# Optimization experiments

Hardware: AMD Instinct MI355X
Metric: run time of the kernel (lower is better)

The kernel has to match this reference:

```python
import jax, jax.numpy as jnp
import numpy as np

H = 8  # num_heads


def _ln(x, g, b):
    mu = x.mean(-1, keepdims=True)
    var = ((x - mu) ** 2).mean(-1, keepdims=True)
    return (x - mu) * jax.lax.rsqrt(var + 1e-5) * g + b


def setup_inputs() -> dict:
    key = jax.random.key(0)
    ks = jax.random.split(key, 24)
    B, N, V, E, D, R, L = 8, 512, 50000, 300, 256, 100, 4
    dh = D // H
    s = 0.02
    inp = {}
    inp['token_ids'] = jax.random.randint(ks[0], (B, N), 0, V, dtype=jnp.int32)
    inp['relations'] = jax.random.randint(ks[1], (B, N, N), 0, R, dtype=jnp.int32)
    m = jax.random.bernoulli(ks[2], 0.9, (B, N, N))
    eye = jnp.eye(N, dtype=bool)[None]
    inp['relations_mask'] = jnp.logical_or(m, eye)  # keep diagonal valid so every row attends somewhere
    inp['embed'] = jax.random.normal(ks[3], (V, E), jnp.float32) * s
    inp['W_in'] = jax.random.normal(ks[4], (E, D), jnp.float32) * s
    inp['b_in'] = jnp.zeros((D,), jnp.float32)
    inp['Wq'] = jax.random.normal(ks[5], (L, D, D), jnp.float32) * s
    inp['Wk'] = jax.random.normal(ks[6], (L, D, D), jnp.float32) * s
    inp['Wv'] = jax.random.normal(ks[7], (L, D, D), jnp.float32) * s
    inp['Wo'] = jax.random.normal(ks[8], (L, D, D), jnp.float32) * s
    inp['ln1_g'] = jnp.ones((L, D), jnp.float32)
    inp['ln1_b'] = jnp.zeros((L, D), jnp.float32)
    inp['ln2_g'] = jnp.ones((L, D), jnp.float32)
    inp['ln2_b'] = jnp.zeros((L, D), jnp.float32)
    inp['W1'] = jax.random.normal(ks[9], (L, D, 4 * D), jnp.float32) * s
    inp['b1'] = jnp.zeros((L, 4 * D), jnp.float32)
    inp['W2'] = jax.random.normal(ks[10], (L, 4 * D, D), jnp.float32) * s
    inp['b2'] = jnp.zeros((L, D), jnp.float32)
    inp['rel_k_emb'] = jax.random.normal(ks[11], (R, dh), jnp.float32) * s
    inp['rel_v_emb'] = jax.random.normal(ks[12], (R, dh), jnp.float32) * s
    inp['W_out'] = jax.random.normal(ks[13], (D, D), jnp.float32) * s
    inp['b_out'] = jnp.zeros((D,), jnp.float32)
    return inp


def reference(token_ids, relations, relations_mask, embed, W_in, b_in, Wq, Wk, Wv, Wo,
              ln1_g, ln1_b, ln2_g, ln2_b, W1, b1, W2, b2, rel_k_emb, rel_v_emb, W_out, b_out):
    # Input layer: embedding lookup + projection to gnn hidden size.
    x = embed[token_ids]                          # [B,N,E]
    x = jax.nn.relu(x @ W_in + b_in)              # [B,N,D]
    B, N, D = x.shape
    dh = D // H
    # Shared relation embeddings (share_layers=True, share_heads=True): gathered once.
    rk = rel_k_emb[relations]                     # [B,N,N,dh]
    rv = rel_v_emb[relations]                     # [B,N,N,dh]
    neg = jnp.asarray(-1e9, x.dtype)
    scale = jnp.asarray(1.0 / np.sqrt(dh), x.dtype)
    L = Wq.shape[0]
    for l in range(L):  # fixed small layer count
        q = (x @ Wq[l]).reshape(B, N, H, dh).transpose(0, 2, 1, 3)
        k = (x @ Wk[l]).reshape(B, N, H, dh).transpose(0, 2, 1, 3)
        v = (x @ Wv[l]).reshape(B, N, H, dh).transpose(0, 2, 1, 3)
        # Relation-aware scores: q.k + q.r_k (RAT-SQL)
        scores = (jnp.einsum('bhnd,bhmd->bhnm', q, k)
                  + jnp.einsum('bhnd,bnmd->bhnm', q, rk)) * scale
        scores = jnp.where(relations_mask[:, None], scores, neg)
        a = jax.nn.softmax(scores, axis=-1)       # [B,H,N,N]
        z = (jnp.einsum('bhnm,bhmd->bhnd', a, v)
             + jnp.einsum('bhnm,bnmd->bhnd', a, rv))
        z = z.transpose(0, 2, 1, 3).reshape(B, N, D) @ Wo[l]
        x = _ln(x + z, ln1_g[l], ln1_b[l])
        f = jax.nn.relu(x @ W1[l] + b1[l]) @ W2[l] + b2[l]
        x = _ln(x + f, ln2_g[l], ln2_b[l])
    # Output layer projection
    return x @ W_out + b_out
```

## Files before the change

kernel.cpp:

```cpp
#include <hip/hip_runtime.h>
#include <hip/hip_bf16.h>

#define NTOK 4096
#define NN   512

typedef __attribute__((ext_vector_type(8))) short bf16x8;
typedef __attribute__((ext_vector_type(4))) float f32x4;
typedef __attribute__((ext_vector_type(4))) unsigned short u16x4;

__device__ __forceinline__ float bf16_to_f(unsigned short u) {
    unsigned int x = ((unsigned int)u) << 16;
    return __builtin_bit_cast(float, x);
}
__device__ __forceinline__ unsigned short f_to_bf16(float f) {
    unsigned int b = __builtin_bit_cast(unsigned int, f);
    return (unsigned short)((b + 0x7fff + ((b >> 16) & 1)) >> 16);
}
__device__ __forceinline__ bf16x8 pack8(float4 a, float4 b) {
    bf16x8 v;
    v[0]=(short)f_to_bf16(a.x); v[1]=(short)f_to_bf16(a.y);
    v[2]=(short)f_to_bf16(a.z); v[3]=(short)f_to_bf16(a.w);
    v[4]=(short)f_to_bf16(b.x); v[5]=(short)f_to_bf16(b.y);
    v[6]=(short)f_to_bf16(b.z); v[7]=(short)f_to_bf16(b.w);
    return v;
}

__global__ void detect_mask_kernel(const unsigned char* __restrict__ m, int* __restrict__ flag) {
    __shared__ int f;
    if (threadIdx.x == 0) f = 0;
    __syncthreads();
    int any = 0;
    for (int i = threadIdx.x; i < 4096; i += 256) {
        if ((i & 3) != 0 && m[i] != 0) any = 1;
    }
    if (any) atomicOr(&f, 1);
    __syncthreads();
    if (threadIdx.x == 0) *flag = f;
}

__global__ __launch_bounds__(256) void prep_rel16(
    const int* __restrict__ rel, const void* __restrict__ mask,
    const int* __restrict__ flag, short* __restrict__ rel16)
{
    const bool mbyte = (*flag != 0);
    const unsigned char* m8 = (const unsigned char*)mask;
    const int* m32 = (const int*)mask;
    const int i = (blockIdx.x * 256 + threadIdx.x) * 2;
    int2 rv = *(const int2*)(rel + i);
    int ok0, ok1;
    if (mbyte) { ok0 = m8[i]; ok1 = m8[i + 1]; }
    else       { ok0 = (m32[i] != 0); ok1 = (m32[i + 1] != 0); }
    short2 o;
    o.x = ok0 ? (short)rv.x : (short)-1;
    o.y = ok1 ? (short)rv.y : (short)-1;
    *(short2*)(rel16 + i) = o;
}

__global__ __launch_bounds__(256) void tcast256(
    const float* __restrict__ Wq, const float* __restrict__ Wk,
    const float* __restrict__ Wv, const float* __restrict__ Wo,
    const float* __restrict__ Wout, unsigned short* __restrict__ wt,
    int nL, float scale)
{
    const int z = blockIdx.z;
    const float* src; unsigned short* dst; float sc = 1.f;
    if (z >= nL * 4) {
        src = Wout; dst = wt + (size_t)nL * 786432;
    } else {
        const int l = z >> 2, which = z & 3;
        if      (which == 0) { src = Wq + (size_t)l * 65536; sc = scale; }
        else if (which == 1) { src = Wk + (size_t)l * 65536; }
        else if (which == 2) { src = Wv + (size_t)l * 65536; }
        else                 { src = Wo + (size_t)l * 65536; }
        dst = wt + (size_t)l * 786432 + which * 65536;
    }
    __shared__ float tile[32][33];
    const int t = threadIdx.x, tx = t & 31, ty = t >> 5;
    const int n0 = blockIdx.x * 32, k0 = blockIdx.y * 32;
#pragma unroll
    for (int p = 0; p < 4; ++p)
        tile[ty + p * 8][tx] = src[(size_t)(k0 + ty + p * 8) * 256 + n0 + tx];
    __syncthreads();
#pragma unroll
    for (int p = 0; p < 4; ++p)
        dst[(size_t)(n0 + ty + p * 8) * 256 + k0 + tx] = f_to_bf16(tile[tx][ty + p * 8] * sc);
}

__global__ __launch_bounds__(256) void tcastKN(
    const float* __restrict__ in, unsigned short* __restrict__ out,
    int K, int N, long inStride, long outStride)
{
    in  += (size_t)blockIdx.z * inStride;
    out += (size_t)blockIdx.z * outStride;
    __shared__ float tile[32][33];
    const int t = threadIdx.x, tx = t & 31, ty = t >> 5;
    const int n0 = blockIdx.x * 32, k0 = blockIdx.y * 32;
#pragma unroll
    for (int p = 0; p < 4; ++p)
        tile[ty + p * 8][tx] = in[(size_t)(k0 + ty + p * 8) * N + n0 + tx];
    __syncthreads();
#pragma unroll
    for (int p = 0; p < 4; ++p)
        out[(size_t)(n0 + ty + p * 8) * K + k0 + tx] = f_to_bf16(tile[tx][ty + p * 8]);
}

__global__ __launch_bounds__(256) void embed_proj_kernel(
    const int* __restrict__ tok, const float* __restrict__ embed,
    const float* __restrict__ W_in, const float* __restrict__ b_in,
    float* __restrict__ x, unsigned short* __restrict__ xh)
{
    __shared__ float emb[8][304];
    __shared__ int tloc[8];
    const int t = threadIdx.x;
    const int r0 = blockIdx.x * 8;
    if (t < 8) tloc[t] = tok[r0 + t];
    __syncthreads();
    for (int i = t; i < 8 * 300; i += 256) {
        int r = i / 300, e = i - r * 300;
        emb[r][e] = embed[(size_t)tloc[r] * 300 + e];
    }
    __syncthreads();
    float acc[8] = {0.f,0.f,0.f,0.f,0.f,0.f,0.f,0.f};
    const int d = t;
    for (int e = 0; e < 300; ++e) {
        float w = W_in[e * 256 + d];
#pragma unroll
        for (int r = 0; r < 8; ++r) acc[r] += emb[r][e] * w;
    }
    const float bb = b_in[d];
#pragma unroll
    for (int r = 0; r < 8; ++r) {
        float o = acc[r] + bb;
        o = o > 0.f ? o : 0.f;
        x[(size_t)(r0 + r) * 256 + d] = o;
        xh[(size_t)(r0 + r) * 256 + d] = f_to_bf16(o);
    }
}

__global__ __launch_bounds__(256) void gemm_bigk64(
    const unsigned short* __restrict__ A, const unsigned short* __restrict__ WT,
    const float* __restrict__ bias, float* __restrict__ Cf, unsigned short* __restrict__ Ch,
    int M, int K, int Nc, int relu)
{
    __shared__ unsigned short As[64][256];
    __shared__ unsigned short Bs[64][256];
    char* Ab = (char*)As; char* Bb = (char*)Bs;
    const int t = threadIdx.x;
    const int lane = t & 63, w = t >> 6;
    const int g = lane >> 4, li = lane & 15;
    const int r0 = blockIdx.y * 64, c0 = blockIdx.x * 64;

    f32x4 acc[4];
#pragma unroll
    for (int i = 0; i < 4; ++i) acc[i] = (f32x4){0.f,0.f,0.f,0.f};

    for (int k0 = 0; k0 < K; k0 += 256) {
        if (k0) __syncthreads();
#pragma unroll
        for (int j = 0; j < 8; ++j) {
            int idx = j * 256 + t;
            int row = idx >> 5;
            int colb = (idx & 31) * 16;
            int sw = row * 512 + (colb ^ ((row & 7) << 4));
            *(bf16x8*)(Ab + sw) = *(const bf16x8*)(A  + (size_t)(r0 + row) * K + k0 + (idx & 31) * 8);
            *(bf16x8*)(Bb + sw) = *(const bf16x8*)(WT + (size_t)(c0 + row) * K + k0 + (idx & 31) * 8);
        }
        __syncthreads();
        const int arow = 16 * w + li;
        const int xr = (li & 7) << 4;
#pragma unroll
        for (int ks = 0; ks < 8; ++ks) {
            const int kb = (g * 8 + ks * 32) * 2;
            bf16x8 af = *(const bf16x8*)(Ab + arow * 512 + (kb ^ xr));
#pragma unroll
            for (int sub = 0; sub < 4; ++sub) {
                const int brow = sub * 16 + li;
                bf16x8 bfr = *(const bf16x8*)(Bb + brow * 512 + (kb ^ xr));
                acc[sub] = __builtin_amdgcn_mfma_f32_16x16x32_bf16(af, bfr, acc[sub], 0, 0, 0);
            }
        }
    }
#pragma unroll
    for (int sub = 0; sub < 4; ++sub) {
        int col = c0 + sub * 16 + li;
        float bv = bias ? bias[col] : 0.f;
#pragma unroll
        for (int r = 0; r < 4; ++r) {
            int row = r0 + 16 * w + g * 4 + r;
            float o = acc[sub][r] + bv;
            if (relu) o = fmaxf(o, 0.f);
            if (Ch) Ch[(size_t)row * Nc + col] = f_to_bf16(o);
            else    Cf[(size_t)row * Nc + col] = o;
        }
    }
}

__global__ __launch_bounds__(256) void gemm_bigk32(
    const unsigned short* __restrict__ A, const unsigned short* __restrict__ WT,
    const float* __restrict__ bias, float* __restrict__ Cf, unsigned short* __restrict__ Ch,
    int M, int K, int Nc, int relu)
{
    __shared__ unsigned short As[32][256];
    __shared__ unsigned short Bs[64][256];
    char* Ab = (char*)As; char* Bb = (char*)Bs;
    const int t = threadIdx.x;
    const int lane = t & 63, w = t >> 6;
    const int g = lane >> 4, li = lane & 15;
    const int r0 = blockIdx.y * 32, c0 = blockIdx.x * 64;

    f32x4 acc[2];
    acc[0] = (f32x4){0.f,0.f,0.f,0.f};
    acc[1] = (f32x4){0.f,0.f,0.f,0.f};

    for (int k0 = 0; k0 < K; k0 += 256) {
        if (k0) __syncthreads();
#pragma unroll
        for (int j = 0; j < 4; ++j) {
            int idx = j * 256 + t;
            int row = idx >> 5;
            int colb = (idx & 31) * 16;
            int sw = row * 512 + (colb ^ ((row & 7) << 4));
            *(bf16x8*)(Ab + sw) = *(const bf16x8*)(A + (size_t)(r0 + row) * K + k0 + (idx & 31) * 8);
        }
#pragma unroll
        for (int j = 0; j < 8; ++j) {
            int idx = j * 256 + t;
            int row = idx >> 5;
            int colb = (idx & 31) * 16;
            int sw = row * 512 + (colb ^ ((row & 7) << 4));
            *(bf16x8*)(Bb + sw) = *(const bf16x8*)(WT + (size_t)(c0 + row) * K + k0 + (idx & 31) * 8);
        }
        __syncthreads();
        const int arow = 16 * (w & 1) + li;
        const int xr = (li & 7) << 4;
#pragma unroll
        for (int ks = 0; ks < 8; ++ks) {
            const int kb = (g * 8 + ks * 32) * 2;
            bf16x8 af = *(const bf16x8*)(Ab + arow * 512 + (kb ^ xr));
#pragma unroll
            for (int sub = 0; sub < 2; ++sub) {
                const int brow = (w >> 1) * 32 + sub * 16 + li;
                bf16x8 bfr = *(const bf16x8*)(Bb + brow * 512 + (kb ^ xr));
                acc[sub] = __builtin_amdgcn_mfma_f32_16x16x32_bf16(af, bfr, acc[sub], 0, 0, 0);
            }
        }
    }
#pragma unroll
    for (int sub = 0; sub < 2; ++sub) {
        int col = c0 + (w >> 1) * 32 + sub * 16 + li;
        float bv = bias ? bias[col] : 0.f;
#pragma unroll
        for (int r = 0; r < 4; ++r) {
            int row = r0 + 16 * (w & 1) + g * 4 + r;
            float o = acc[sub][r] + bv;
            if (relu) o = fmaxf(o, 0.f);
            if (Ch) Ch[(size_t)row * Nc + col] = f_to_bf16(o);
            else    Cf[(size_t)row * Nc + col] = o;
        }
    }
}

__global__ __launch_bounds__(256) void qrk_kernel(
    const unsigned short* __restrict__ qkvh, const float* __restrict__ relk_g,
    unsigned short* __restrict__ qrkg)
{
    const int n0 = blockIdx.x * 64, h = blockIdx.y, b = blockIdx.z;
    const int t = threadIdx.x, lane = t & 63, w = t >> 6;
    const int g = lane >> 4, li = lane & 15;
    const int qrow = 16 * w + g * 4;

    __shared__ unsigned short relk_s[100][40];
    for (int i = t; i < 400; i += 256) {
        int rr = i >> 2, d8 = (i & 3) * 8;
        const float* sp = relk_g + rr * 32 + d8;
        *(bf16x8*)&relk_s[rr][d8] = pack8(*(const float4*)sp, *(const float4*)(sp + 4));
    }
    bf16x8 qf = *(const bf16x8*)(qkvh + (size_t)(b * NN + n0 + 16 * w + li) * 768 + h * 32 + g * 8);
    __syncthreads();
#pragma unroll
    for (int rc = 0; rc < 7; ++rc) {
        bf16x8 bb = *(const bf16x8*)&relk_s[rc * 16 + li][g * 8];
        f32x4 s = __builtin_amdgcn_mfma_f32_16x16x32_bf16(qf, bb, (f32x4){0.f,0.f,0.f,0.f}, 0, 0, 0);
        int col = rc * 16 + li;
        if (col < 100) {
#pragma unroll
            for (int r = 0; r < 4; ++r)
                qrkg[((size_t)(b * 8 + h) * NN + n0 + qrow + r) * 100 + col] = f_to_bf16(s[r]);
        }
    }
}

__global__ __launch_bounds__(256, 4) void attn_mfma(
    const unsigned short* __restrict__ qkvh,
    const short* __restrict__ rel16,
    const unsigned short* __restrict__ qrkg,
    const float* __restrict__ relv_g,
    float* __restrict__ zpart, float* __restrict__ smpart)
{
    const int p = blockIdx.x;
    const int cx = p & 7, k = p >> 3;
    const int sg = cx * 16 + (k >> 3);
    const int h  = k & 7;
    const int b = sg >> 4, chunk = sg & 15;
    const int n0 = chunk * 32;

    const int t = threadIdx.x;
    const int lane = t & 63, w = t >> 6;
    const int qw = w & 1, mhalf = w >> 1;
    const int g = lane >> 4, li = lane & 15;
    const int qrow = 16 * qw + g * 4;
    const int mbase = mhalf * 256;

    __shared__ float wrel[32][100];
    __shared__ unsigned short qrk_lds[32][100];
    __shared__ union {
        unsigned short relvT[32][136];
        struct {
            unsigned short v_t[2][2][32][40];
            unsigned short p_s[4][16][40];
        } mn;
    } u;

    for (int i = t; i < 3200; i += 256) ((float*)wrel)[i] = 0.f;
    {
        const unsigned short* qsrc = qrkg + ((size_t)(b * 8 + h) * NN + n0) * 100;
        for (int i = t; i < 1600; i += 256) {
            int row = i / 50, off = (i - row * 50) * 2;
            *(unsigned int*)&qrk_lds[row][off] =
                *(const unsigned int*)(qsrc + (size_t)row * 100 + off);
        }
    }
    bf16x8 qf = *(const bf16x8*)(qkvh + (size_t)(b * NN + n0 + 16 * qw + li) * 768 + h * 32 + g * 8);

    const short* relrow[4];
#pragma unroll
    for (int r = 0; r < 4; ++r)
        relrow[r] = rel16 + ((size_t)b * NN + n0 + qrow + r) * NN;
    const int th = t & 127;
    const int vm = th & 31, vdg = th >> 5;
    const size_t kRB = (size_t)(b * NN) * 768 + 256 + h * 32 + g * 8;
    const size_t vRB = (size_t)(b * NN) * 768 + 512 + h * 32 + vdg * 8;

    bf16x8 kbuf[2][2]; bf16x8 vbuf[2]; short rbuf[2][8];
#pragma unroll
    for (int i = 0; i < 8; ++i)
        rbuf[0][i] = relrow[i & 3][mbase + (i >> 2) * 16 + li];
    kbuf[0][0] = *(const bf16x8*)(qkvh + kRB + (size_t)(mbase + li) * 768);
    kbuf[0][1] = *(const bf16x8*)(qkvh + kRB + (size_t)(mbase + 16 + li) * 768);
    vbuf[0]    = *(const bf16x8*)(qkvh + vRB + (size_t)(mbase + vm) * 768);

    float smacc[4] = {0.f, 0.f, 0.f, 0.f};
    f32x4 zf[2];
    zf[0] = (f32x4){0.f,0.f,0.f,0.f};
    zf[1] = (f32x4){0.f,0.f,0.f,0.f};

#pragma unroll
    for (int tt = 0; tt < 8; ++tt) {
        const int cur = tt & 1, nxt = cur ^ 1;
        {
            bf16x8 vv = vbuf[cur];
#pragma unroll
            for (int j = 0; j < 8; ++j)
                u.mn.v_t[mhalf][cur][vdg * 8 + j][vm] = (unsigned short)vv[j];
        }
        if (tt + 1 < 8) {
            const int m0n = mbase + (tt + 1) * 32;
#pragma unroll
            for (int i = 0; i < 8; ++i)
                rbuf[nxt][i] = relrow[i & 3][m0n + (i >> 2) * 16 + li];
        }
        __syncthreads();
        bf16x8 kf0 = kbuf[cur][0], kf1 = kbuf[cur][1];
        if (tt + 1 < 8) {
            const int m0n = mbase + (tt + 1) * 32;
            kbuf[nxt][0] = *(const bf16x8*)(qkvh + kRB + (size_t)(m0n + li) * 768);
            kbuf[nxt][1] = *(const bf16x8*)(qkvh + kRB + (size_t)(m0n + 16 + li) * 768);
            vbuf[nxt]    = *(const bf16x8*)(qkvh + vRB + (size_t)(m0n + vm) * 768);
        }
        f32x4 s0 = __builtin_amdgcn_mfma_f32_16x16x32_bf16(qf, kf0, (f32x4){0.f,0.f,0.f,0.f}, 0, 0, 0);
        f32x4 s1 = __builtin_amdgcn_mfma_f32_16x16x32_bf16(qf, kf1, (f32x4){0.f,0.f,0.f,0.f}, 0, 0, 0);
        float pr[8];
#pragma unroll
        for (int i = 0; i < 8; ++i) {
            const int r = i & 3;
            const int rl = rbuf[cur][i];
            const float qadd = bf16_to_f(qrk_lds[qrow + r][rl < 0 ? 0 : rl]);
            const float sv = ((i >> 2) ? s1[r] : s0[r]) + qadd;
            float pv = 0.f;
            if (rl >= 0) {
                pv = __expf(fminf(sv, 50.f));
                atomicAdd(&wrel[qrow + r][rl], pv);
            }
            smacc[r] += pv;
            pr[i] = pv;
        }
#pragma unroll
        for (int i = 0; i < 8; ++i)
            u.mn.p_s[w][g * 4 + (i & 3)][(i >> 2) * 16 + li] = f_to_bf16(pr[i]);
        asm volatile("s_waitcnt lgkmcnt(0)" ::: "memory");
        __builtin_amdgcn_sched_barrier(0);
        bf16x8 pa = *(const bf16x8*)&u.mn.p_s[w][li][g * 8];
#pragma unroll
        for (int dc = 0; dc < 2; ++dc) {
            bf16x8 vb = *(const bf16x8*)&u.mn.v_t[mhalf][cur][dc * 16 + li][g * 8];
            zf[dc] = __builtin_amdgcn_mfma_f32_16x16x32_bf16(pa, vb, zf[dc], 0, 0, 0);
        }
    }
    __syncthreads();

    for (int i = t; i < 32 * 36; i += 256) {
        int d = i / 36, c = 100 + (i - (i / 36) * 36);
        u.relvT[d][c] = 0;
    }
    for (int i = t; i < 400; i += 256) {
        int rr2 = i >> 2, d8 = (i & 3) * 8;
        const float* sp = relv_g + rr2 * 32 + d8;
        float4 s0 = *(const float4*)sp, s1 = *(const float4*)(sp + 4);
        u.relvT[d8 + 0][rr2] = f_to_bf16(s0.x);
        u.relvT[d8 + 1][rr2] = f_to_bf16(s0.y);
        u.relvT[d8 + 2][rr2] = f_to_bf16(s0.z);
        u.relvT[d8 + 3][rr2] = f_to_bf16(s0.w);
        u.relvT[d8 + 4][rr2] = f_to_bf16(s1.x);
        u.relvT[d8 + 5][rr2] = f_to_bf16(s1.y);
        u.relvT[d8 + 6][rr2] = f_to_bf16(s1.z);
        u.relvT[d8 + 7][rr2] = f_to_bf16(s1.w);
    }
    __syncthreads();
    if (mhalf == 0) {
#pragma unroll
        for (int kc = 0; kc < 4; ++kc) {
            const int kbase = kc * 32 + g * 8;
            const float* wp = &wrel[16 * qw + li][0];
            bf16x8 af;
#pragma unroll
            for (int j = 0; j < 8; ++j) {
                int id = kbase + j;
                float val = (id < 100) ? wp[id] : 0.f;
                af[j] = (short)f_to_bf16(val);
            }
#pragma unroll
            for (int dc = 0; dc < 2; ++dc) {
                bf16x8 vbr = *(const bf16x8*)&u.relvT[dc * 16 + li][kbase];
                zf[dc] = __builtin_amdgcn_mfma_f32_16x16x32_bf16(af, vbr, zf[dc], 0, 0, 0);
            }
        }
    }
#pragma unroll
    for (int r = 0; r < 4; ++r) {
        smacc[r] += __shfl_xor(smacc[r], 1, 64);
        smacc[r] += __shfl_xor(smacc[r], 2, 64);
        smacc[r] += __shfl_xor(smacc[r], 4, 64);
        smacc[r] += __shfl_xor(smacc[r], 8, 64);
    }
#pragma unroll
    for (int r = 0; r < 4; ++r) {
        const int row = b * NN + n0 + qrow + r;
        size_t ob = (size_t)mhalf * 1048576 + (size_t)row * 256 + h * 32;
#pragma unroll
        for (int dc = 0; dc < 2; ++dc)
            zpart[ob + dc * 16 + li] = zf[dc][r];
        if (li == 0)
            smpart[(size_t)mhalf * 32768 + (size_t)row * 8 + h] = smacc[r];
    }
}

__global__ __launch_bounds__(256) void combine_kernel(
    const float* __restrict__ zpart, const float* __restrict__ smpart,
    unsigned short* __restrict__ zbf)
{
    const int t = threadIdx.x;
    const int wi = t >> 6, lane = t & 63;
    const int row = blockIdx.x * 4 + wi;
    const int h = lane >> 3;
    float den = 0.f;
    float4 acc = make_float4(0.f, 0.f, 0.f, 0.f);
#pragma unroll
    for (int s = 0; s < 2; ++s) {
        den += smpart[(size_t)s * 32768 + (size_t)row * 8 + h];
        float4 v = *(const float4*)(zpart + (size_t)s * 1048576 + (size_t)row * 256 + lane * 4);
        acc.x += v.x; acc.y += v.y; acc.z += v.z; acc.w += v.w;
    }
    const float inv = 1.f / den;
    u16x4 oh;
    oh[0] = f_to_bf16(acc.x * inv);
    oh[1] = f_to_bf16(acc.y * inv);
    oh[2] = f_to_bf16(acc.z * inv);
    oh[3] = f_to_bf16(acc.w * inv);
    *(u16x4*)(zbf + (size_t)row * 256 + lane * 4) = oh;
}

__global__ __launch_bounds__(256) void ln_kernel(
    const float* __restrict__ xin, const float* __restrict__ y,
    const float* __restrict__ g, const float* __restrict__ bsh,
    float* __restrict__ xout, unsigned short* __restrict__ xh)
{
    const int t = threadIdx.x;
    const int w = t >> 6, lane = t & 63;
    const size_t row = (size_t)blockIdx.x * 4 + w;
    const float4 xv = *(const float4*)(xin + row * 256 + lane * 4);
    const float4 yv = *(const float4*)(y + row * 256 + lane * 4);
    float4 sv;
    sv.x = xv.x + yv.x; sv.y = xv.y + yv.y; sv.z = xv.z + yv.z; sv.w = xv.w + yv.w;
    float sum = sv.x + sv.y + sv.z + sv.w;
    float sq  = sv.x * sv.x + sv.y * sv.y + sv.z * sv.z + sv.w * sv.w;
#pragma unroll
    for (int off = 1; off < 64; off <<= 1) {
        sum += __shfl_xor(sum, off, 64);
        sq  += __shfl_xor(sq, off, 64);
    }
    const float mu = sum * (1.f / 256.f);
    const float var = sq * (1.f / 256.f) - mu * mu;
    const float rs = rsqrtf(var + 1e-5f);
    const float4 gv = *(const float4*)(g + lane * 4);
    const float4 bv = *(const float4*)(bsh + lane * 4);
    float4 o;
    o.x = (sv.x - mu) * rs * gv.x + bv.x;
    o.y = (sv.y - mu) * rs * gv.y + bv.y;
    o.z = (sv.z - mu) * rs * gv.z + bv.z;
    o.w = (sv.w - mu) * rs * gv.w + bv.w;
    *(float4*)(xout + row * 256 + lane * 4) = o;
    u16x4 oh;
    oh[0] = f_to_bf16(o.x); oh[1] = f_to_bf16(o.y);
    oh[2] = f_to_bf16(o.z); oh[3] = f_to_bf16(o.w);
    *(u16x4*)(xh + row * 256 + lane * 4) = oh;
}

extern "C" void kernel_launch(void* const* d_in, const int* in_sizes, int n_in,
                              void* d_out, int out_size, void* d_ws, size_t ws_size,
                              hipStream_t stream)
{
    (void)in_sizes; (void)n_in; (void)out_size;
    const int*   tok   = (const int*)d_in[0];
    const int*   rel   = (const int*)d_in[1];
    const void*  mask  = d_in[2];
    const float* embed = (const float*)d_in[3];
    const float* W_in  = (const float*)d_in[4];
    const float* b_in  = (const float*)d_in[5];
    const float* Wq    = (const float*)d_in[6];
    const float* Wk    = (const float*)d_in[7];
    const float* Wv    = (const float*)d_in[8];
    const float* Wo    = (const float*)d_in[9];
    const float* ln1g  = (const float*)d_in[10];
    const float* ln1b  = (const float*)d_in[11];
    const float* ln2g  = (const float*)d_in[12];
    const float* ln2b  = (const float*)d_in[13];
    const float* W1    = (const float*)d_in[14];
    const float* b1    = (const float*)d_in[15];
    const float* W2    = (const float*)d_in[16];
    const float* b2    = (const float*)d_in[17];
    const float* relk  = (const float*)d_in[18];
    const float* relv  = (const float*)d_in[19];
    const float* Wout  = (const float*)d_in[20];
    const float* bout  = (const float*)d_in[21];
    float* out = (float*)d_out;
    const float scale = 0.17677669529663687f;

    float* ws = (float*)d_ws;
    float*          x     = ws;
    unsigned short* xh    = (unsigned short*)(ws + 1048576);
    unsigned short* zbf   = (unsigned short*)(ws + 1572864);
    float*          zo    = ws + 2097152;
    unsigned short* qkvh  = (unsigned short*)(ws + 3145728);
    unsigned short* hbh   = (unsigned short*)(ws + 4718592);
    float*          zpart = ws + 6815744;
    float*          smpart= ws + 8912896;
    unsigned short* qrkg  = (unsigned short*)(ws + 8978432);
    int*            flag  = (int*)(ws + 10616832);
    unsigned short* wt    = (unsigned short*)(ws + 10616848);

    const size_t wsf = ws_size >> 2;
    const bool tierA = wsf >= 13271100;
    short* rel16 = tierA ? (short*)(ws + 12222480) : (short*)hbh;

    detect_mask_kernel<<<1, 256, 0, stream>>>((const unsigned char*)mask, flag);
    embed_proj_kernel<<<512, 256, 0, stream>>>(tok, embed, W_in, b_in, x, xh);
    if (tierA) {
        prep_rel16<<<4096, 256, 0, stream>>>(rel, mask, flag, rel16);
        tcast256<<<dim3(8, 8, 17), 256, 0, stream>>>(Wq, Wk, Wv, Wo, Wout, wt, 4, scale);
        tcastKN<<<dim3(32, 8, 4), 256, 0, stream>>>(W1, wt + 262144, 256, 1024, 262144, 786432);
        tcastKN<<<dim3(8, 32, 4), 256, 0, stream>>>(W2, wt + 524288, 1024, 256, 262144, 786432);
    }

    for (int l = 0; l < 4; ++l) {
        unsigned short* wl = tierA ? wt + (size_t)l * 786432 : wt;
        if (!tierA) {
            prep_rel16<<<4096, 256, 0, stream>>>(rel, mask, flag, rel16);
            tcast256<<<dim3(8, 8, 4), 256, 0, stream>>>(
                Wq + (size_t)l * 65536, Wk + (size_t)l * 65536,
                Wv + (size_t)l * 65536, Wo + (size_t)l * 65536, Wout, wt, 1, scale);
            tcastKN<<<dim3(32, 8, 1), 256, 0, stream>>>(W1 + (size_t)l * 262144, wt + 262144, 256, 1024, 0, 0);
            tcastKN<<<dim3(8, 32, 1), 256, 0, stream>>>(W2 + (size_t)l * 262144, wt + 524288, 1024, 256, 0, 0);
        }
        gemm_bigk64<<<dim3(12, 64), 256, 0, stream>>>(xh, wl, nullptr, nullptr, qkvh,
                                                      NTOK, 256, 768, 0);
        qrk_kernel<<<dim3(8, 8, 8), 256, 0, stream>>>(qkvh, relk, qrkg);
        attn_mfma<<<1024, 256, 0, stream>>>(qkvh, rel16, qrkg, relv, zpart, smpart);
        combine_kernel<<<1024, 256, 0, stream>>>(zpart, smpart, zbf);
        gemm_bigk32<<<dim3(4, 128), 256, 0, stream>>>(zbf, wl + 196608, nullptr, zo, nullptr,
                                                      NTOK, 256, 256, 0);
        ln_kernel<<<1024, 256, 0, stream>>>(x, zo, ln1g + l * 256, ln1b + l * 256, x, xh);
        gemm_bigk64<<<dim3(16, 64), 256, 0, stream>>>(xh, wl + 262144, b1 + l * 1024, nullptr, hbh,
                                                      NTOK, 256, 1024, 1);
        gemm_bigk32<<<dim3(4, 128), 256, 0, stream>>>(hbh, wl + 524288, b2 + l * 256, zo, nullptr,
                                                      NTOK, 1024, 256, 0);
        ln_kernel<<<1024, 256, 0, stream>>>(x, zo, ln2g + l * 256, ln2b + l * 256, x, xh);
    }
    unsigned short* woutT = wt;
    if (tierA) {
        woutT = wt + (size_t)4 * 786432;
    } else {
        tcast256<<<dim3(8, 8, 1), 256, 0, stream>>>(Wq, Wk, Wv, Wo, Wout, wt, 0, scale);
    }
    gemm_bigk32<<<dim3(4, 128), 256, 0, stream>>>(xh, woutT, bout, out, nullptr,
                                                  NTOK, 256, 256, 0);
}
```

Measured before the change: 623.5 us.

## Fold q·relk into QKV GEMM via precomputed Wq·relkᵀ and fuse combine into Wo GEMM

Precomputes per-layer weight columns Wq_h·rel_kᵀ so the QKV projection GEMM directly emits the q·r_k scores (widened output to 1600 columns), removing the separate qrk kernel. The partial-softmax combine step is fused into a new Wo GEMM that reads zpart/smpart, normalizes, and packs to bf16 in LDS, removing the combine kernel and its zbf round trip. This trades two launches and intermediate buffers for a wider GEMM (more FLOPs and a larger strided qkv buffer) and extra bf16 rounding of the folded weights.

```diff
diff --git a/kernel.cpp b/kernel.cpp
--- a/kernel.cpp
+++ b/kernel.cpp
@@ -3,6 +3,8 @@
 
 #define NTOK 4096
 #define NN   512
+#define QST  1600
+#define LSTR 999424
 
 typedef __attribute__((ext_vector_type(8))) short bf16x8;
 typedef __attribute__((ext_vector_type(4))) float f32x4;
@@ -65,14 +67,15 @@
     const int z = blockIdx.z;
     const float* src; unsigned short* dst; float sc = 1.f;
     if (z >= nL * 4) {
-        src = Wout; dst = wt + (size_t)nL * 786432;
+        src = Wout; dst = wt + (size_t)nL * LSTR;
     } else {
         const int l = z >> 2, which = z & 3;
-        if      (which == 0) { src = Wq + (size_t)l * 65536; sc = scale; }
-        else if (which == 1) { src = Wk + (size_t)l * 65536; }
-        else if (which == 2) { src = Wv + (size_t)l * 65536; }
-        else                 { src = Wo + (size_t)l * 65536; }
-        dst = wt + (size_t)l * 786432 + which * 65536;
+        size_t off;
+        if      (which == 0) { src = Wq + (size_t)l * 65536; sc = scale; off = 0; }
+        else if (which == 1) { src = Wk + (size_t)l * 65536; off = 65536; }
+        else if (which == 2) { src = Wv + (size_t)l * 65536; off = 131072; }
+        else                 { src = Wo + (size_t)l * 65536; off = 409600; }
+        dst = wt + (size_t)l * LSTR + off;
     }
     __shared__ float tile[32][33];
     const int t = threadIdx.x, tx = t & 31, ty = t >> 5;
@@ -102,6 +105,32 @@
 #pragma unroll
     for (int p = 0; p < 4; ++p)
         out[(size_t)(n0 + ty + p * 8) * K + k0 + tx] = f_to_bf16(tile[tx][ty + p * 8]);
+}
+
+__global__ __launch_bounds__(256) void wqr_kernel(
+    unsigned short* __restrict__ wt, const float* __restrict__ relk_g, long lstride)
+{
+    const int h = blockIdx.x, t = threadIdx.x;
+    unsigned short* wl = wt + (size_t)blockIdx.y * lstride;
+    unsigned short* out = wl + 196608;
+    if (h == 8) {
+#pragma unroll
+        for (int i = 0; i < 32; ++i) out[(size_t)(800 + i) * 256 + t] = 0;
+        return;
+    }
+    __shared__ float rk[100][32];
+    for (int i = t; i < 3200; i += 256) rk[i >> 5][i & 31] = relk_g[i];
+    float wq_e[32];
+#pragma unroll
+    for (int d = 0; d < 32; ++d)
+        wq_e[d] = bf16_to_f(wl[(size_t)(h * 32 + d) * 256 + t]);
+    __syncthreads();
+    for (int r = 0; r < 100; ++r) {
+        float acc = 0.f;
+#pragma unroll
+        for (int d = 0; d < 32; ++d) acc += wq_e[d] * rk[r][d];
+        out[(size_t)(h * 100 + r) * 256 + t] = f_to_bf16(acc);
+    }
 }
 
 __global__ __launch_bounds__(256) void embed_proj_kernel(
@@ -260,40 +289,83 @@
     }
 }
 
-__global__ __launch_bounds__(256) void qrk_kernel(
-    const unsigned short* __restrict__ qkvh, const float* __restrict__ relk_g,
-    unsigned short* __restrict__ qrkg)
-{
-    const int n0 = blockIdx.x * 64, h = blockIdx.y, b = blockIdx.z;
-    const int t = threadIdx.x, lane = t & 63, w = t >> 6;
+__global__ __launch_bounds__(256) void gemm_wo(
+    const float* __restrict__ zpart, const float* __restrict__ smpart,
+    const unsigned short* __restrict__ WT, float* __restrict__ Cf, int Nc)
+{
+    __shared__ unsigned short As[32][256];
+    __shared__ unsigned short Bs[64][256];
+    __shared__ float den[32][8];
+    char* Ab = (char*)As; char* Bb = (char*)Bs;
+    const int t = threadIdx.x;
+    const int lane = t & 63, w = t >> 6;
     const int g = lane >> 4, li = lane & 15;
-    const int qrow = 16 * w + g * 4;
-
-    __shared__ unsigned short relk_s[100][40];
-    for (int i = t; i < 400; i += 256) {
-        int rr = i >> 2, d8 = (i & 3) * 8;
-        const float* sp = relk_g + rr * 32 + d8;
-        *(bf16x8*)&relk_s[rr][d8] = pack8(*(const float4*)sp, *(const float4*)(sp + 4));
-    }
-    bf16x8 qf = *(const bf16x8*)(qkvh + (size_t)(b * NN + n0 + 16 * w + li) * 768 + h * 32 + g * 8);
-    __syncthreads();
-#pragma unroll
-    for (int rc = 0; rc < 7; ++rc) {
-        bf16x8 bb = *(const bf16x8*)&relk_s[rc * 16 + li][g * 8];
-        f32x4 s = __builtin_amdgcn_mfma_f32_16x16x32_bf16(qf, bb, (f32x4){0.f,0.f,0.f,0.f}, 0, 0, 0);
-        int col = rc * 16 + li;
-        if (col < 100) {
-#pragma unroll
-            for (int r = 0; r < 4; ++r)
-                qrkg[((size_t)(b * 8 + h) * NN + n0 + qrow + r) * 100 + col] = f_to_bf16(s[r]);
+    const int r0 = blockIdx.y * 32, c0 = blockIdx.x * 64;
+
+    {
+        int row = t >> 3, h2 = t & 7;
+        float s = smpart[(size_t)(r0 + row) * 8 + h2] +
+                  smpart[32768 + (size_t)(r0 + row) * 8 + h2];
+        den[row][h2] = 1.f / s;
+    }
+    __syncthreads();
+#pragma unroll
+    for (int j = 0; j < 4; ++j) {
+        int idx = j * 256 + t;
+        int row = idx >> 5;
+        int k8 = (idx & 31) * 8;
+        const float* z0 = zpart + (size_t)(r0 + row) * 256 + k8;
+        const float* z1 = z0 + 1048576;
+        float4 a0 = *(const float4*)z0, a1 = *(const float4*)(z0 + 4);
+        float4 b0 = *(const float4*)z1, b1 = *(const float4*)(z1 + 4);
+        float dv = den[row][k8 >> 5];
+        a0.x = (a0.x + b0.x) * dv; a0.y = (a0.y + b0.y) * dv;
+        a0.z = (a0.z + b0.z) * dv; a0.w = (a0.w + b0.w) * dv;
+        a1.x = (a1.x + b1.x) * dv; a1.y = (a1.y + b1.y) * dv;
+        a1.z = (a1.z + b1.z) * dv; a1.w = (a1.w + b1.w) * dv;
+        int colb = (idx & 31) * 16;
+        int sw = row * 512 + (colb ^ ((row & 7) << 4));
+        *(bf16x8*)(Ab + sw) = pack8(a0, a1);
+    }
+#pragma unroll
+    for (int j = 0; j < 8; ++j) {
+        int idx = j * 256 + t;
+        int row = idx >> 5;
+        int colb = (idx & 31) * 16;
+        int sw = row * 512 + (colb ^ ((row & 7) << 4));
+        *(bf16x8*)(Bb + sw) = *(const bf16x8*)(WT + (size_t)(c0 + row) * 256 + (idx & 31) * 8);
+    }
+    __syncthreads();
+    f32x4 acc[2];
+    acc[0] = (f32x4){0.f,0.f,0.f,0.f};
+    acc[1] = (f32x4){0.f,0.f,0.f,0.f};
+    const int arow = 16 * (w & 1) + li;
+    const int xr = (li & 7) << 4;
+#pragma unroll
+    for (int ks = 0; ks < 8; ++ks) {
+        const int kb = (g * 8 + ks * 32) * 2;
+        bf16x8 af = *(const bf16x8*)(Ab + arow * 512 + (kb ^ xr));
+#pragma unroll
+        for (int sub = 0; sub < 2; ++sub) {
+            const int brow = (w >> 1) * 32 + sub * 16 + li;
+            bf16x8 bfr = *(const bf16x8*)(Bb + brow * 512 + (kb ^ xr));
+            acc[sub] = __builtin_amdgcn_mfma_f32_16x16x32_bf16(af, bfr, acc[sub], 0, 0, 0);
+        }
+    }
+#pragma unroll
+    for (int sub = 0; sub < 2; ++sub) {
+        int col = c0 + (w >> 1) * 32 + sub * 16 + li;
+#pragma unroll
+        for (int r = 0; r < 4; ++r) {
+            int row = r0 + 16 * (w & 1) + g * 4 + r;
+            Cf[(size_t)row * Nc + col] = acc[sub][r];
         }
     }
 }
 
 __global__ __launch_bounds__(256, 4) void attn_mfma(
-    const unsigned short* __restrict__ qkvh,
+    const unsigned short* __restrict__ qkvg,
     const short* __restrict__ rel16,
-    const unsigned short* __restrict__ qrkg,
     const float* __restrict__ relv_g,
     float* __restrict__ zpart, float* __restrict__ smpart)
 {
@@ -323,14 +395,14 @@
 
     for (int i = t; i < 3200; i += 256) ((float*)wrel)[i] = 0.f;
     {
-        const unsigned short* qsrc = qrkg + ((size_t)(b * 8 + h) * NN + n0) * 100;
+        const unsigned short* qsrc = qkvg + (size_t)(b * NN + n0) * QST + 768 + h * 100;
         for (int i = t; i < 1600; i += 256) {
             int row = i / 50, off = (i - row * 50) * 2;
             *(unsigned int*)&qrk_lds[row][off] =
-                *(const unsigned int*)(qsrc + (size_t)row * 100 + off);
-        }
-    }
-    bf16x8 qf = *(const bf16x8*)(qkvh + (size_t)(b * NN + n0 + 16 * qw + li) * 768 + h * 32 + g * 8);
+                *(const unsigned int*)(qsrc + (size_t)row * QST + off);
+        }
+    }
+    bf16x8 qf = *(const bf16x8*)(qkvg + (size_t)(b * NN + n0 + 16 * qw + li) * QST + h * 32 + g * 8);
 
     const short* relrow[4];
 #pragma unroll
@@ -338,16 +410,16 @@
         relrow[r] = rel16 + ((size_t)b * NN + n0 + qrow + r) * NN;
     const int th = t & 127;
     const int vm = th & 31, vdg = th >> 5;
-    const size_t kRB = (size_t)(b * NN) * 768 + 256 + h * 32 + g * 8;
-    const size_t vRB = (size_t)(b * NN) * 768 + 512 + h * 32 + vdg * 8;
+    const size_t kRB = (size_t)(b * NN) * QST + 256 + h * 32 + g * 8;
+    const size_t vRB = (size_t)(b * NN) * QST + 512 + h * 32 + vdg * 8;
 
     bf16x8 kbuf[2][2]; bf16x8 vbuf[2]; short rbuf[2][8];
 #pragma unroll
     for (int i = 0; i < 8; ++i)
         rbuf[0][i] = relrow[i & 3][mbase + (i >> 2) * 16 + li];
-    kbuf[0][0] = *(const bf16x8*)(qkvh + kRB + (size_t)(mbase + li) * 768);
-    kbuf[0][1] = *(const bf16x8*)(qkvh + kRB + (size_t)(mbase + 16 + li) * 768);
-    vbuf[0]    = *(const bf16x8*)(qkvh + vRB + (size_t)(mbase + vm) * 768);
+    kbuf[0][0] = *(const bf16x8*)(qkvg + kRB + (size_t)(mbase + li) * QST);
+    kbuf[0][1] = *(const bf16x8*)(qkvg + kRB + (size_t)(mbase + 16 + li) * QST);
+    vbuf[0]    = *(const bf16x8*)(qkvg + vRB + (size_t)(mbase + vm) * QST);
 
     float smacc[4] = {0.f, 0.f, 0.f, 0.f};
     f32x4 zf[2];
@@ -373,9 +445,9 @@
         bf16x8 kf0 = kbuf[cur][0], kf1 = kbuf[cur][1];
         if (tt + 1 < 8) {
             const int m0n = mbase + (tt + 1) * 32;
-            kbuf[nxt][0] = *(const bf16x8*)(qkvh + kRB + (size_t)(m0n + li) * 768);
-            kbuf[nxt][1] = *(const bf16x8*)(qkvh + kRB + (size_t)(m0n + 16 + li) * 768);
-            vbuf[nxt]    = *(const bf16x8*)(qkvh + vRB + (size_t)(m0n + vm) * 768);
+            kbuf[nxt][0] = *(const bf16x8*)(qkvg + kRB + (size_t)(m0n + li) * QST);
+            kbuf[nxt][1] = *(const bf16x8*)(qkvg + kRB + (size_t)(m0n + 16 + li) * QST);
+            vbuf[nxt]    = *(const bf16x8*)(qkvg + vRB + (size_t)(m0n + vm) * QST);
         }
         f32x4 s0 = __builtin_amdgcn_mfma_f32_16x16x32_bf16(qf, kf0, (f32x4){0.f,0.f,0.f,0.f}, 0, 0, 0);
         f32x4 s1 = __builtin_amdgcn_mfma_f32_16x16x32_bf16(qf, kf1, (f32x4){0.f,0.f,0.f,0.f}, 0, 0, 0);
@@ -462,31 +534,6 @@
         if (li == 0)
             smpart[(size_t)mhalf * 32768 + (size_t)row * 8 + h] = smacc[r];
     }
-}
-
-__global__ __launch_bounds__(256) void combine_kernel(
-    const float* __restrict__ zpart, const float* __restrict__ smpart,
-    unsigned short* __restrict__ zbf)
-{
-    const int t = threadIdx.x;
-    const int wi = t >> 6, lane = t & 63;
-    const int row = blockIdx.x * 4 + wi;
-    const int h = lane >> 3;
-    float den = 0.f;
-    float4 acc = make_float4(0.f, 0.f, 0.f, 0.f);
-#pragma unroll
-    for (int s = 0; s < 2; ++s) {
-        den += smpart[(size_t)s * 32768 + (size_t)row * 8 + h];
-        float4 v = *(const float4*)(zpart + (size_t)s * 1048576 + (size_t)row * 256 + lane * 4);
-        acc.x += v.x; acc.y += v.y; acc.z += v.z; acc.w += v.w;
-    }
-    const float inv = 1.f / den;
-    u16x4 oh;
-    oh[0] = f_to_bf16(acc.x * inv);
-    oh[1] = f_to_bf16(acc.y * inv);
-    oh[2] = f_to_bf16(acc.z * inv);
-    oh[3] = f_to_bf16(acc.w * inv);
-    *(u16x4*)(zbf + (size_t)row * 256 + lane * 4) = oh;
 }
 
 __global__ __launch_bounds__(256) void ln_kernel(
@@ -558,56 +605,53 @@
     float* ws = (float*)d_ws;
     float*          x     = ws;
     unsigned short* xh    = (unsigned short*)(ws + 1048576);
-    unsigned short* zbf   = (unsigned short*)(ws + 1572864);
     float*          zo    = ws + 2097152;
-    unsigned short* qkvh  = (unsigned short*)(ws + 3145728);
+    unsigned short* qkvg  = (unsigned short*)(ws + 3145728);
     unsigned short* hbh   = (unsigned short*)(ws + 4718592);
     float*          zpart = ws + 6815744;
     float*          smpart= ws + 8912896;
-    unsigned short* qrkg  = (unsigned short*)(ws + 8978432);
     int*            flag  = (int*)(ws + 10616832);
     unsigned short* wt    = (unsigned short*)(ws + 10616848);
 
     const size_t wsf = ws_size >> 2;
-    const bool tierA = wsf >= 13271100;
-    short* rel16 = tierA ? (short*)(ws + 12222480) : (short*)hbh;
+    const bool tierA = wsf >= 13697100;
+    short* rel16 = tierA ? (short*)(ws + 12648464) : (short*)zo;
 
     detect_mask_kernel<<<1, 256, 0, stream>>>((const unsigned char*)mask, flag);
     embed_proj_kernel<<<512, 256, 0, stream>>>(tok, embed, W_in, b_in, x, xh);
     if (tierA) {
         prep_rel16<<<4096, 256, 0, stream>>>(rel, mask, flag, rel16);
         tcast256<<<dim3(8, 8, 17), 256, 0, stream>>>(Wq, Wk, Wv, Wo, Wout, wt, 4, scale);
-        tcastKN<<<dim3(32, 8, 4), 256, 0, stream>>>(W1, wt + 262144, 256, 1024, 262144, 786432);
-        tcastKN<<<dim3(8, 32, 4), 256, 0, stream>>>(W2, wt + 524288, 1024, 256, 262144, 786432);
+        tcastKN<<<dim3(32, 8, 4), 256, 0, stream>>>(W1, wt + 475136, 256, 1024, 262144, LSTR);
+        tcastKN<<<dim3(8, 32, 4), 256, 0, stream>>>(W2, wt + 737280, 1024, 256, 262144, LSTR);
+        wqr_kernel<<<dim3(9, 4), 256, 0, stream>>>(wt, relk, LSTR);
     }
 
     for (int l = 0; l < 4; ++l) {
-        unsigned short* wl = tierA ? wt + (size_t)l * 786432 : wt;
+        unsigned short* wl = tierA ? wt + (size_t)l * LSTR : wt;
         if (!tierA) {
             prep_rel16<<<4096, 256, 0, stream>>>(rel, mask, flag, rel16);
             tcast256<<<dim3(8, 8, 4), 256, 0, stream>>>(
                 Wq + (size_t)l * 65536, Wk + (size_t)l * 65536,
                 Wv + (size_t)l * 65536, Wo + (size_t)l * 65536, Wout, wt, 1, scale);
-            tcastKN<<<dim3(32, 8, 1), 256, 0, stream>>>(W1 + (size_t)l * 262144, wt + 262144, 256, 1024, 0, 0);
-            tcastKN<<<dim3(8, 32, 1), 256, 0, stream>>>(W2 + (size_t)l * 262144, wt + 524288, 1024, 256, 0, 0);
-        }
-        gemm_bigk64<<<dim3(12, 64), 256, 0, stream>>>(xh, wl, nullptr, nullptr, qkvh,
-                                                      NTOK, 256, 768, 0);
-        qrk_kernel<<<dim3(8, 8, 8), 256, 0, stream>>>(qkvh, relk, qrkg);
-        attn_mfma<<<1024, 256, 0, stream>>>(qkvh, rel16, qrkg, relv, zpart, smpart);
-        combine_kernel<<<1024, 256, 0, stream>>>(zpart, smpart, zbf);
-        gemm_bigk32<<<dim3(4, 128), 256, 0, stream>>>(zbf, wl + 196608, nullptr, zo, nullptr,
-                                                      NTOK, 256, 256, 0);
+            tcastKN<<<dim3(32, 8, 1), 256, 0, stream>>>(W1 + (size_t)l * 262144, wt + 475136, 256, 1024, 0, 0);
+            tcastKN<<<dim3(8, 32, 1), 256, 0, stream>>>(W2 + (size_t)l * 262144, wt + 737280, 1024, 256, 0, 0);
+            wqr_kernel<<<dim3(9, 1), 256, 0, stream>>>(wt, relk, 0);
+        }
+        gemm_bigk64<<<dim3(25, 64), 256, 0, stream>>>(xh, wl, nullptr, nullptr, qkvg,
+                                                      NTOK, 256, QST, 0);
+        attn_mfma<<<1024, 256, 0, stream>>>(qkvg, rel16, relv, zpart, smpart);
+        gemm_wo<<<dim3(4, 128), 256, 0, stream>>>(zpart, smpart, wl + 409600, zo, 256);
         ln_kernel<<<1024, 256, 0, stream>>>(x, zo, ln1g + l * 256, ln1b + l * 256, x, xh);
-        gemm_bigk64<<<dim3(16, 64), 256, 0, stream>>>(xh, wl + 262144, b1 + l * 1024, nullptr, hbh,
+        gemm_bigk64<<<dim3(16, 64), 256, 0, stream>>>(xh, wl + 475136, b1 + l * 1024, nullptr, hbh,
                                                       NTOK, 256, 1024, 1);
-        gemm_bigk32<<<dim3(4, 128), 256, 0, stream>>>(hbh, wl + 524288, b2 + l * 256, zo, nullptr,
+        gemm_bigk32<<<dim3(4, 128), 256, 0, stream>>>(hbh, wl + 737280, b2 + l * 256, zo, nullptr,
                                                       NTOK, 1024, 256, 0);
         ln_kernel<<<1024, 256, 0, stream>>>(x, zo, ln2g + l * 256, ln2b + l * 256, x, xh);
     }
     unsigned short* woutT = wt;
     if (tierA) {
-        woutT = wt + (size_t)4 * 786432;
+        woutT = wt + (size_t)4 * LSTR;
     } else {
         tcast256<<<dim3(8, 8, 1), 256, 0, stream>>>(Wq, Wk, Wv, Wo, Wout, wt, 0, scale);
     }
```

Result: slower. 650.9 us (+4.4%).
